# Kernel tuning notes

Hardware: AMD Instinct MI355X
Metric: run time of the kernel (lower is better)

## Reference

```python
import jax, jax.numpy as jnp
import numpy as np

T, N, H, G = 4, 100000, 128, 1024
LN2 = float(np.log(2.0))
EPS = 1e-5


def ssp(x):
    # shifted softplus: softplus(x) - softplus(0)
    return jax.nn.softplus(x) - LN2


def layernorm(x, g, b):
    m = jnp.mean(x, axis=-1, keepdims=True)
    v = jnp.var(x, axis=-1, keepdims=True)
    return (x - m) * jax.lax.rsqrt(v + EPS) * g + b


def mlp3(x, Ws, bs, gs, bts):
    # 3 stacked Linear -> LayerNorm -> SSP stages
    for i in range(3):
        x = ssp(layernorm(x @ Ws[i] + bs[i], gs[i], bts[i]))
    return x


def setup_inputs() -> dict:
    key = jax.random.key(0)
    ks = jax.random.split(key, 8)
    s = 1.0 / np.sqrt(H)
    batch = jnp.sort((jnp.arange(N, dtype=jnp.int64) * G) // N).astype(jnp.int32)
    return {
        "x_proc": jax.random.normal(ks[0], (T, N, H), jnp.float32),
        "x_enc": jax.random.normal(ks[1], (N, H), jnp.float32),
        "batch": batch,
        "pW": jax.random.normal(ks[2], (3, H, H), jnp.float32) * s,
        "pb": jnp.zeros((3, H), jnp.float32),
        "pg": jnp.ones((3, H), jnp.float32),
        "pbt": jnp.zeros((3, H), jnp.float32),
        "eW": jax.random.normal(ks[3], (3, H, H), jnp.float32) * s,
        "eb": jnp.zeros((3, H), jnp.float32),
        "eg": jnp.ones((3, H), jnp.float32),
        "ebt": jnp.zeros((3, H), jnp.float32),
        "wp": jax.random.normal(ks[4], (H, 1), jnp.float32) * s,
        "bp": jnp.zeros((1,), jnp.float32),
        "we": jax.random.normal(ks[5], (H, 1), jnp.float32) * s,
        "be": jnp.zeros((1,), jnp.float32),
    }


def reference(x_proc, x_enc, batch, pW, pb, pg, pbt, eW, eb, eg, ebt, wp, bp, we, be):
    h_proc = mlp3(x_proc, pW, pb, pg, pbt)          # [T, N, H]
    h_enc = mlp3(x_enc, eW, eb, eg, ebt)            # [N, H]
    seg = lambda z: jax.ops.segment_sum(z, batch, num_segments=G)
    pooled_proc = jax.vmap(seg)(h_proc)             # [T, G, H]
    pooled_enc = seg(h_enc)                         # [G, H]
    target = pooled_proc @ wp + bp + (pooled_enc @ we + be)[None]  # [T, G, 1]
    return target.reshape(-1, G)                    # [T, G]
```

## Files before the change

### kernel.cpp

```cpp
#include <hip/hip_runtime.h>
#include <hip/hip_bf16.h>

typedef unsigned short u16;
typedef unsigned int u32;
typedef __bf16 bf16x8 __attribute__((ext_vector_type(8)));
typedef float f32x16 __attribute__((ext_vector_type(16)));
typedef float f32x4 __attribute__((ext_vector_type(4)));
typedef float f32x2 __attribute__((ext_vector_type(2)));
typedef u32 u32x4 __attribute__((ext_vector_type(4)));

typedef struct { f32x2 h[2]; } f32x4p;
typedef struct { f32x2 h[8]; } f32x16p;

typedef __attribute__((address_space(1))) const u32 glb_u32;
typedef __attribute__((address_space(3))) u32 lds_u32;

#define NN 100000
#define NPROC_BLOCKS 3125
#define NENC_BLOCKS 782
#define LN2F 0.69314718055994530942f
#define LOG2EF 1.44269504088896340736f
#define CSTRIDE 1284

__device__ __forceinline__ u16 f2bf(float f) {
  u32 u = __float_as_uint(f);
  u32 r = u + 0x7fffu + ((u >> 16) & 1u);
  return (u16)(r >> 16);
}

__device__ __forceinline__ u32 pk2(float a, float b) {
  float2 f2; f2.x = a; f2.y = b;
  __hip_bfloat162 h = __float22bfloat162_rn(f2);
  u32 r;
  __builtin_memcpy(&r, &h, 4);
  return r;
}

__device__ __forceinline__ float l2p1e(float xp) {
  return __builtin_amdgcn_logf(1.0f + __builtin_amdgcn_exp2f(xp));
}

__global__ void prep_kernel(const float* __restrict__ pW, const float* __restrict__ eW,
                            const float* __restrict__ pb, const float* __restrict__ pg,
                            const float* __restrict__ pbt,
                            const float* __restrict__ eb, const float* __restrict__ eg,
                            const float* __restrict__ ebt,
                            const float* __restrict__ wp, const float* __restrict__ we,
                            const float* __restrict__ bp, const float* __restrict__ be,
                            u16* __restrict__ wt, float* __restrict__ cprep,
                            float* __restrict__ out) {
  int bx = blockIdx.x;
  int t = threadIdx.x;
  if (bx < 384) {
    int idx = bx * 256 + t;
    int m = idx >> 14;
    int within = idx & 16383;
    int r = within >> 7;
    int c = within & 127;
    int k = (((c >> 3) ^ (r & 15)) << 3) | (c & 7);
    const float* src = (m < 3) ? pW : eW;
    int ms = (m < 3) ? m : m - 3;
    float w = src[ms * 16384 + k * 128 + r];
    if (ms >= 1) w *= LN2F;
    wt[idx] = f2bf(w);
    if (idx < 4096) out[idx] = bp[0] + be[0];
  } else {
    int which = bx - 384;
    int net = which / 3;
    int s = which % 3;
    const float* W  = net ? eW : pW;
    const float* b  = net ? eb : pb;
    const float* g  = net ? eg : pg;
    const float* bt = net ? ebt : pbt;
    const float* wv = net ? we : wp;
    float* cp = cprep + net * CSTRIDE;
    __shared__ float red[128];

    int j = t & 127;
    int half = t >> 7;
    if (t < 128) {
      cp[(s * 3 + 1) * 128 + j] = g[s * 128 + j] * LOG2EF;
      cp[(s * 3 + 2) * 128 + j] = bt[s * 128 + j] * LOG2EF;
    }
    if (s == 0) {
      if (t < 128) {
        cp[0 * 128 + j] = b[j];
        cp[9 * 128 + j] = LN2F * wv[j];
      }
      if (t < 64) {
        float v = wv[t] + wv[t + 64];
        #pragma unroll
        for (int off = 1; off < 64; off <<= 1) v += __shfl_xor(v, off, 64);
        if (t == 0) cp[1280] = -LN2F * v;
      }
    } else {
      float part = 0.f;
      const float* Ws = W + s * 16384 + half * 64 * 128 + j;
      #pragma unroll 8
      for (int k = 0; k < 64; ++k) part += Ws[k * 128];
      if (half == 1) red[j] = part;
      __syncthreads();
      if (half == 0) {
        float cs = part + red[j];
        cp[(s * 3 + 0) * 128 + j] = b[s * 128 + j] - LN2F * cs;
      }
    }
  }
}

__global__ __launch_bounds__(256, 3)
void mlp_kernel(const float* __restrict__ x_proc, const float* __restrict__ x_enc,
                const u16* __restrict__ wt, const float* __restrict__ cprep,
                const int* __restrict__ batch, float* __restrict__ out) {
  __shared__ __align__(16) unsigned char wbuf[32768];
  __shared__ f32x4 cball[10][32];
  __shared__ float c0s;

  const bool is_proc = blockIdx.x < NPROC_BLOCKS;
  const int bid2 = is_proc ? blockIdx.x : blockIdx.x - NPROC_BLOCKS;
  const float* x = is_proc ? x_proc : x_enc;
  const unsigned char* wgb = (const unsigned char*)(is_proc ? wt : wt + 49152);
  const float* cp = cprep + (is_proc ? 0 : CSTRIDE);
  const int nrows = is_proc ? 400000 : 100000;

  const int tid = threadIdx.x;
  const int lane = tid & 63;
  const int wid = tid >> 6;
  const int l31 = lane & 31;
  const u32 hi = (u32)(lane >> 5);
  const int brow = bid2 * 128;

  auto issue_w = [&](int s_) {
    #pragma unroll
    for (int i = 0; i < 8; ++i) {
      const unsigned char* gp = wgb + s_ * 32768 + i * 4096 + tid * 16;
      unsigned char* lp = wbuf + i * 4096 + wid * 1024;
      __builtin_amdgcn_global_load_lds((const glb_u32*)(const void*)gp,
                                       (lds_u32*)(void*)lp, 16, 0, 0);
    }
  };

  issue_w(0);

  for (int i = tid; i < 320; i += 256)
    ((f32x4*)cball)[i] = *(const f32x4*)(cp + i * 4);
  if (tid == 0) c0s = cp[1280];

  const int rloc = wid * 32 + l31;
  const int grow = brow + rloc;
  const float* xr = x + (size_t)((grow < nrows) ? grow : (nrows - 1)) * 128 + (int)hi * 8;
  bf16x8 bfr[8];
  {
    f32x4 a[16];
    #pragma unroll
    for (int ks = 0; ks < 8; ++ks) {
      a[2 * ks]     = *(const f32x4*)(xr + ks * 16);
      a[2 * ks + 1] = *(const f32x4*)(xr + ks * 16 + 4);
    }
    #pragma unroll
    for (int ks = 0; ks < 8; ++ks) {
      u32x4 tq;
      tq.x = pk2(a[2 * ks][0], a[2 * ks][1]);
      tq.y = pk2(a[2 * ks][2], a[2 * ks][3]);
      tq.z = pk2(a[2 * ks + 1][0], a[2 * ks + 1][1]);
      tq.w = pk2(a[2 * ks + 1][2], a[2 * ks + 1][3]);
      bfr[ks] = __builtin_bit_cast(bf16x8, tq);
    }
  }

  float pfin = 0.0f;

  #pragma unroll
  for (int s = 0; s < 3; ++s) {
    __syncthreads();

    f32x16 acc[4];
    #pragma unroll
    for (int jf = 0; jf < 4; ++jf)
      #pragma unroll
      for (int q = 0; q < 4; ++q) {
        f32x4 b4 = cball[s * 3 + 0][jf * 8 + 2 * q + (int)hi];
        acc[jf][4 * q + 0] = b4[0];
        acc[jf][4 * q + 1] = b4[1];
        acc[jf][4 * q + 2] = b4[2];
        acc[jf][4 * q + 3] = b4[3];
      }

    #pragma unroll
    for (int ks = 0; ks < 8; ++ks) {
      int aoff = l31 * 256 + (((2 * ks + (int)hi) ^ (l31 & 15)) << 4);
      #pragma unroll
      for (int jf = 0; jf < 4; ++jf) {
        const bf16x8 afrag = *(const bf16x8*)(const void*)(wbuf + jf * 8192 + aoff);
        acc[jf] = __builtin_amdgcn_mfma_f32_32x32x16_bf16(afrag, bfr[ks], acc[jf], 0, 0, 0);
      }
      if (ks & 1) __builtin_amdgcn_sched_barrier(0);
    }

    if (s < 2) {
      __syncthreads();
      issue_w(s + 1);
    }

    f32x2 s1v = {0.f, 0.f}, s2v = {0.f, 0.f};
    #pragma unroll
    for (int jf = 0; jf < 4; ++jf) {
      f32x16p az = __builtin_bit_cast(f32x16p, acc[jf]);
      f32x2 p1 = {0.f, 0.f}, p2 = {0.f, 0.f};
      #pragma unroll
      for (int e = 0; e < 8; ++e) {
        f32x2 v = az.h[e];
        p1 += v;
        p2 = __builtin_elementwise_fma(v, v, p2);
      }
      s1v += p1; s2v += p2;
    }
    float s1 = s1v[0] + s1v[1];
    float s2 = s2v[0] + s2v[1];
    s1 += __shfl_xor(s1, 32, 64);
    s2 += __shfl_xor(s2, 32, 64);
    float mean = s1 * 0.0078125f;
    float var = s2 * 0.0078125f - mean * mean;
    float rstd = rsqrtf(var + 1e-5f);
    float nmr = -mean * rstd;
    const f32x2 rstd2 = {rstd, rstd};
    const f32x2 nmr2 = {nmr, nmr};

    if (s < 2) {
      #pragma unroll
      for (int ks = 0; ks < 8; ++ks) {
        int jf = ks >> 1, q0 = (ks & 1) << 1;
        f32x16p az = __builtin_bit_cast(f32x16p, acc[jf]);
        uint2 wq[2];
        #pragma unroll
        for (int qq = 0; qq < 2; ++qq) {
          int q = q0 + qq;
          f32x4p g = __builtin_bit_cast(f32x4p, cball[s * 3 + 1][jf * 8 + 2 * q + (int)hi]);
          f32x4p t = __builtin_bit_cast(f32x4p, cball[s * 3 + 2][jf * 8 + 2 * q + (int)hi]);
          f32x2 u0 = __builtin_elementwise_fma(az.h[2 * q + 0], rstd2, nmr2);
          f32x2 u1 = __builtin_elementwise_fma(az.h[2 * q + 1], rstd2, nmr2);
          f32x2 x0 = __builtin_elementwise_fma(u0, g.h[0], t.h[0]);
          f32x2 x1 = __builtin_elementwise_fma(u1, g.h[1], t.h[1]);
          wq[qq].x = pk2(l2p1e(x0[0]), l2p1e(x0[1]));
          wq[qq].y = pk2(l2p1e(x1[0]), l2p1e(x1[1]));
        }
        u32 sx = hi ? wq[0].x : wq[1].x;
        u32 sy = hi ? wq[0].y : wq[1].y;
        u32 rx = (u32)__shfl_xor((int)sx, 32, 64);
        u32 ry = (u32)__shfl_xor((int)sy, 32, 64);
        u32x4 tq;
        tq.x = hi ? rx : wq[0].x;
        tq.y = hi ? ry : wq[0].y;
        tq.z = hi ? wq[1].x : rx;
        tq.w = hi ? wq[1].y : ry;
        bfr[ks] = __builtin_bit_cast(bf16x8, tq);
      }
    } else {
      float pa = 0.f, pb2 = 0.f;
      #pragma unroll
      for (int jf = 0; jf < 4; ++jf) {
        f32x16p az = __builtin_bit_cast(f32x16p, acc[jf]);
        #pragma unroll
        for (int q = 0; q < 4; ++q) {
          f32x4 g4 = cball[7][jf * 8 + 2 * q + (int)hi];
          f32x4 t4 = cball[8][jf * 8 + 2 * q + (int)hi];
          f32x4 w4 = cball[9][jf * 8 + 2 * q + (int)hi];
          f32x4p g = __builtin_bit_cast(f32x4p, g4);
          f32x4p t = __builtin_bit_cast(f32x4p, t4);
          f32x2 u0 = __builtin_elementwise_fma(az.h[2 * q + 0], rstd2, nmr2);
          f32x2 u1 = __builtin_elementwise_fma(az.h[2 * q + 1], rstd2, nmr2);
          f32x2 x0 = __builtin_elementwise_fma(u0, g.h[0], t.h[0]);
          f32x2 x1 = __builtin_elementwise_fma(u1, g.h[1], t.h[1]);
          pa = __builtin_fmaf(l2p1e(x0[0]), w4[0], pa);
          pb2 = __builtin_fmaf(l2p1e(x0[1]), w4[1], pb2);
          pa = __builtin_fmaf(l2p1e(x1[0]), w4[2], pa);
          pb2 = __builtin_fmaf(l2p1e(x1[1]), w4[3], pb2);
        }
      }
      pfin = pa + pb2;
    }
  }

  pfin += __shfl_xor(pfin, 32, 64);
  if (grow < nrows) {
    pfin += c0s;
    int cell;
    if (is_proc) {
      int tt = grow / NN;
      cell = tt * 1024 + batch[grow - tt * NN];
    } else {
      cell = batch[grow];
    }
    int ca = __shfl(cell, 0, 32);
    int cz = __shfl(cell, 31, 32);
    if (ca == cz) {
      float r = pfin;
      #pragma unroll
      for (int off = 1; off < 32; off <<= 1) r += __shfl_xor(r, off, 64);
      if (hi == 0) {
        if (is_proc) {
          if (l31 == 0) atomicAdd(out + ca, r);
        } else {
          if (l31 < 4) atomicAdd(out + l31 * 1024 + ca, r);
        }
      }
    } else if (hi == 0) {
      if (is_proc) {
        atomicAdd(out + cell, pfin);
      } else {
        #pragma unroll
        for (int t2 = 0; t2 < 4; ++t2) atomicAdd(out + t2 * 1024 + cell, pfin);
      }
    }
  }
}

extern "C" void kernel_launch(void* const* d_in, const int* in_sizes, int n_in,
                              void* d_out, int out_size, void* d_ws, size_t ws_size,
                              hipStream_t stream) {
  const float* x_proc = (const float*)d_in[0];
  const float* x_enc  = (const float*)d_in[1];
  const int*   batch  = (const int*)d_in[2];
  const float* pW  = (const float*)d_in[3];
  const float* pb  = (const float*)d_in[4];
  const float* pg  = (const float*)d_in[5];
  const float* pbt = (const float*)d_in[6];
  const float* eW  = (const float*)d_in[7];
  const float* eb  = (const float*)d_in[8];
  const float* eg  = (const float*)d_in[9];
  const float* ebt = (const float*)d_in[10];
  const float* wp  = (const float*)d_in[11];
  const float* bp  = (const float*)d_in[12];
  const float* we  = (const float*)d_in[13];
  const float* be  = (const float*)d_in[14];

  float* out = (float*)d_out;
  u16* wt_ws = (u16*)d_ws;
  float* cprep = (float*)((char*)d_ws + 196608);

  prep_kernel<<<390, 256, 0, stream>>>(pW, eW, pb, pg, pbt, eb, eg, ebt,
                                       wp, we, bp, be, wt_ws, cprep, out);
  mlp_kernel<<<NPROC_BLOCKS + NENC_BLOCKS, 256, 0, stream>>>(
      x_proc, x_enc, wt_ws, cprep, batch, out);
}
```

Baseline: 144.2 us.

## Convert MLP kernel to persistent blocks with atomic tile counter

Launches a fixed number of persistent blocks (768 total, split between proc and enc) that fetch further 128-row tiles through a global atomic counter initialized in the prep kernel. This removes per-block launch overhead and the repeated per-block loading of constants, and balances work dynamically. The stage-0 weight reload is issued at the end of each tile while atomics are done, but x loads for the next tile are not prefetched ahead of compute, so latency may be exposed. It adds an extra global atomic and barrier per tile.

```diff
diff --git a/kernel.cpp b/kernel.cpp
--- a/kernel.cpp
+++ b/kernel.cpp
@@ -16,11 +16,14 @@
 typedef __attribute__((address_space(3))) u32 lds_u32;
 
 #define NN 100000
-#define NPROC_BLOCKS 3125
-#define NENC_BLOCKS 782
+#define NPROC_TILES 3125
+#define NENC_TILES 782
+#define NPROC_PBLK 614
+#define NENC_PBLK 154
 #define LN2F 0.69314718055994530942f
 #define LOG2EF 1.44269504088896340736f
 #define CSTRIDE 1284
+#define CNT_OFF 206880
 
 __device__ __forceinline__ u16 f2bf(float f) {
   u32 u = __float_as_uint(f);
@@ -48,7 +51,7 @@
                             const float* __restrict__ wp, const float* __restrict__ we,
                             const float* __restrict__ bp, const float* __restrict__ be,
                             u16* __restrict__ wt, float* __restrict__ cprep,
-                            float* __restrict__ out) {
+                            int* __restrict__ cnt, float* __restrict__ out) {
   int bx = blockIdx.x;
   int t = threadIdx.x;
   if (bx < 384) {
@@ -64,6 +67,7 @@
     if (ms >= 1) w *= LN2F;
     wt[idx] = f2bf(w);
     if (idx < 4096) out[idx] = bp[0] + be[0];
+    if (bx == 0 && t == 0) { cnt[0] = NPROC_PBLK; cnt[1] = NENC_PBLK; }
   } else {
     int which = bx - 384;
     int net = which / 3;
@@ -111,24 +115,27 @@
 __global__ __launch_bounds__(256, 3)
 void mlp_kernel(const float* __restrict__ x_proc, const float* __restrict__ x_enc,
                 const u16* __restrict__ wt, const float* __restrict__ cprep,
-                const int* __restrict__ batch, float* __restrict__ out) {
+                const int* __restrict__ batch, int* __restrict__ cnt,
+                float* __restrict__ out) {
   __shared__ __align__(16) unsigned char wbuf[32768];
   __shared__ f32x4 cball[10][32];
   __shared__ float c0s;
-
-  const bool is_proc = blockIdx.x < NPROC_BLOCKS;
-  const int bid2 = is_proc ? blockIdx.x : blockIdx.x - NPROC_BLOCKS;
+  __shared__ int sh_tn;
+
+  const bool is_proc = blockIdx.x < NPROC_PBLK;
+  const int bid2 = is_proc ? blockIdx.x : blockIdx.x - NPROC_PBLK;
   const float* x = is_proc ? x_proc : x_enc;
   const unsigned char* wgb = (const unsigned char*)(is_proc ? wt : wt + 49152);
   const float* cp = cprep + (is_proc ? 0 : CSTRIDE);
   const int nrows = is_proc ? 400000 : 100000;
+  const int ntiles = is_proc ? NPROC_TILES : NENC_TILES;
+  int* cntp = cnt + (is_proc ? 0 : 1);
 
   const int tid = threadIdx.x;
   const int lane = tid & 63;
   const int wid = tid >> 6;
   const int l31 = lane & 31;
   const u32 hi = (u32)(lane >> 5);
-  const int brow = bid2 * 128;
 
   auto issue_w = [&](int s_) {
     #pragma unroll
@@ -147,10 +154,12 @@
   if (tid == 0) c0s = cp[1280];
 
   const int rloc = wid * 32 + l31;
-  const int grow = brow + rloc;
-  const float* xr = x + (size_t)((grow < nrows) ? grow : (nrows - 1)) * 128 + (int)hi * 8;
+  int tile = bid2;
+  int grow = tile * 128 + rloc;
+
   bf16x8 bfr[8];
-  {
+  auto load_x = [&]() {
+    const float* xr = x + (size_t)((grow < nrows) ? grow : (nrows - 1)) * 128 + (int)hi * 8;
     f32x4 a[16];
     #pragma unroll
     for (int ks = 0; ks < 8; ++ks) {
@@ -166,152 +175,165 @@
       tq.w = pk2(a[2 * ks + 1][2], a[2 * ks + 1][3]);
       bfr[ks] = __builtin_bit_cast(bf16x8, tq);
     }
-  }
-
-  float pfin = 0.0f;
-
-  #pragma unroll
-  for (int s = 0; s < 3; ++s) {
-    __syncthreads();
-
-    f32x16 acc[4];
+  };
+  load_x();
+
+  for (;;) {
+    float pfin = 0.0f;
+
     #pragma unroll
-    for (int jf = 0; jf < 4; ++jf)
+    for (int s = 0; s < 3; ++s) {
+      __syncthreads();
+      if (s == 2 && tid == 0) sh_tn = atomicAdd(cntp, 1);
+
+      f32x16 acc[4];
       #pragma unroll
-      for (int q = 0; q < 4; ++q) {
-        f32x4 b4 = cball[s * 3 + 0][jf * 8 + 2 * q + (int)hi];
-        acc[jf][4 * q + 0] = b4[0];
-        acc[jf][4 * q + 1] = b4[1];
-        acc[jf][4 * q + 2] = b4[2];
-        acc[jf][4 * q + 3] = b4[3];
-      }
-
-    #pragma unroll
-    for (int ks = 0; ks < 8; ++ks) {
-      int aoff = l31 * 256 + (((2 * ks + (int)hi) ^ (l31 & 15)) << 4);
-      #pragma unroll
-      for (int jf = 0; jf < 4; ++jf) {
-        const bf16x8 afrag = *(const bf16x8*)(const void*)(wbuf + jf * 8192 + aoff);
-        acc[jf] = __builtin_amdgcn_mfma_f32_32x32x16_bf16(afrag, bfr[ks], acc[jf], 0, 0, 0);
-      }
-      if (ks & 1) __builtin_amdgcn_sched_barrier(0);
-    }
-
-    if (s < 2) {
-      __syncthreads();
-      issue_w(s + 1);
-    }
-
-    f32x2 s1v = {0.f, 0.f}, s2v = {0.f, 0.f};
-    #pragma unroll
-    for (int jf = 0; jf < 4; ++jf) {
-      f32x16p az = __builtin_bit_cast(f32x16p, acc[jf]);
-      f32x2 p1 = {0.f, 0.f}, p2 = {0.f, 0.f};
-      #pragma unroll
-      for (int e = 0; e < 8; ++e) {
-        f32x2 v = az.h[e];
-        p1 += v;
-        p2 = __builtin_elementwise_fma(v, v, p2);
-      }
-      s1v += p1; s2v += p2;
-    }
-    float s1 = s1v[0] + s1v[1];
-    float s2 = s2v[0] + s2v[1];
-    s1 += __shfl_xor(s1, 32, 64);
-    s2 += __shfl_xor(s2, 32, 64);
-    float mean = s1 * 0.0078125f;
-    float var = s2 * 0.0078125f - mean * mean;
-    float rstd = rsqrtf(var + 1e-5f);
-    float nmr = -mean * rstd;
-    const f32x2 rstd2 = {rstd, rstd};
-    const f32x2 nmr2 = {nmr, nmr};
-
-    if (s < 2) {
+      for (int jf = 0; jf < 4; ++jf)
+        #pragma unroll
+        for (int q = 0; q < 4; ++q) {
+          f32x4 b4 = cball[s * 3 + 0][jf * 8 + 2 * q + (int)hi];
+          acc[jf][4 * q + 0] = b4[0];
+          acc[jf][4 * q + 1] = b4[1];
+          acc[jf][4 * q + 2] = b4[2];
+          acc[jf][4 * q + 3] = b4[3];
+        }
+
       #pragma unroll
       for (int ks = 0; ks < 8; ++ks) {
-        int jf = ks >> 1, q0 = (ks & 1) << 1;
-        f32x16p az = __builtin_bit_cast(f32x16p, acc[jf]);
-        uint2 wq[2];
-        #pragma unroll
-        for (int qq = 0; qq < 2; ++qq) {
-          int q = q0 + qq;
-          f32x4p g = __builtin_bit_cast(f32x4p, cball[s * 3 + 1][jf * 8 + 2 * q + (int)hi]);
-          f32x4p t = __builtin_bit_cast(f32x4p, cball[s * 3 + 2][jf * 8 + 2 * q + (int)hi]);
-          f32x2 u0 = __builtin_elementwise_fma(az.h[2 * q + 0], rstd2, nmr2);
-          f32x2 u1 = __builtin_elementwise_fma(az.h[2 * q + 1], rstd2, nmr2);
-          f32x2 x0 = __builtin_elementwise_fma(u0, g.h[0], t.h[0]);
-          f32x2 x1 = __builtin_elementwise_fma(u1, g.h[1], t.h[1]);
-          wq[qq].x = pk2(l2p1e(x0[0]), l2p1e(x0[1]));
-          wq[qq].y = pk2(l2p1e(x1[0]), l2p1e(x1[1]));
-        }
-        u32 sx = hi ? wq[0].x : wq[1].x;
-        u32 sy = hi ? wq[0].y : wq[1].y;
-        u32 rx = (u32)__shfl_xor((int)sx, 32, 64);
-        u32 ry = (u32)__shfl_xor((int)sy, 32, 64);
-        u32x4 tq;
-        tq.x = hi ? rx : wq[0].x;
-        tq.y = hi ? ry : wq[0].y;
-        tq.z = hi ? wq[1].x : rx;
-        tq.w = hi ? wq[1].y : ry;
-        bfr[ks] = __builtin_bit_cast(bf16x8, tq);
-      }
-    } else {
-      float pa = 0.f, pb2 = 0.f;
+        int aoff = l31 * 256 + (((2 * ks + (int)hi) ^ (l31 & 15)) << 4);
+        #pragma unroll
+        for (int jf = 0; jf < 4; ++jf) {
+          const bf16x8 afrag = *(const bf16x8*)(const void*)(wbuf + jf * 8192 + aoff);
+          acc[jf] = __builtin_amdgcn_mfma_f32_32x32x16_bf16(afrag, bfr[ks], acc[jf], 0, 0, 0);
+        }
+        if (ks & 1) __builtin_amdgcn_sched_barrier(0);
+      }
+
+      if (s < 2) {
+        __syncthreads();
+        issue_w(s + 1);
+      }
+
+      f32x2 s1v = {0.f, 0.f}, s2v = {0.f, 0.f};
       #pragma unroll
       for (int jf = 0; jf < 4; ++jf) {
         f32x16p az = __builtin_bit_cast(f32x16p, acc[jf]);
-        #pragma unroll
-        for (int q = 0; q < 4; ++q) {
-          f32x4 g4 = cball[7][jf * 8 + 2 * q + (int)hi];
-          f32x4 t4 = cball[8][jf * 8 + 2 * q + (int)hi];
-          f32x4 w4 = cball[9][jf * 8 + 2 * q + (int)hi];
-          f32x4p g = __builtin_bit_cast(f32x4p, g4);
-          f32x4p t = __builtin_bit_cast(f32x4p, t4);
-          f32x2 u0 = __builtin_elementwise_fma(az.h[2 * q + 0], rstd2, nmr2);
-          f32x2 u1 = __builtin_elementwise_fma(az.h[2 * q + 1], rstd2, nmr2);
-          f32x2 x0 = __builtin_elementwise_fma(u0, g.h[0], t.h[0]);
-          f32x2 x1 = __builtin_elementwise_fma(u1, g.h[1], t.h[1]);
-          pa = __builtin_fmaf(l2p1e(x0[0]), w4[0], pa);
-          pb2 = __builtin_fmaf(l2p1e(x0[1]), w4[1], pb2);
-          pa = __builtin_fmaf(l2p1e(x1[0]), w4[2], pa);
-          pb2 = __builtin_fmaf(l2p1e(x1[1]), w4[3], pb2);
-        }
-      }
-      pfin = pa + pb2;
-    }
-  }
-
-  pfin += __shfl_xor(pfin, 32, 64);
-  if (grow < nrows) {
-    pfin += c0s;
-    int cell;
-    if (is_proc) {
-      int tt = grow / NN;
-      cell = tt * 1024 + batch[grow - tt * NN];
-    } else {
-      cell = batch[grow];
-    }
-    int ca = __shfl(cell, 0, 32);
-    int cz = __shfl(cell, 31, 32);
-    if (ca == cz) {
-      float r = pfin;
-      #pragma unroll
-      for (int off = 1; off < 32; off <<= 1) r += __shfl_xor(r, off, 64);
-      if (hi == 0) {
+        f32x2 p1 = {0.f, 0.f}, p2 = {0.f, 0.f};
+        #pragma unroll
+        for (int e = 0; e < 8; ++e) {
+          f32x2 v = az.h[e];
+          p1 += v;
+          p2 = __builtin_elementwise_fma(v, v, p2);
+        }
+        s1v += p1; s2v += p2;
+      }
+      float s1 = s1v[0] + s1v[1];
+      float s2 = s2v[0] + s2v[1];
+      s1 += __shfl_xor(s1, 32, 64);
+      s2 += __shfl_xor(s2, 32, 64);
+      float mean = s1 * 0.0078125f;
+      float var = s2 * 0.0078125f - mean * mean;
+      float rstd = rsqrtf(var + 1e-5f);
+      float nmr = -mean * rstd;
+      const f32x2 rstd2 = {rstd, rstd};
+      const f32x2 nmr2 = {nmr, nmr};
+
+      if (s < 2) {
+        #pragma unroll
+        for (int ks = 0; ks < 8; ++ks) {
+          int jf = ks >> 1, q0 = (ks & 1) << 1;
+          f32x16p az = __builtin_bit_cast(f32x16p, acc[jf]);
+          uint2 wq[2];
+          #pragma unroll
+          for (int qq = 0; qq < 2; ++qq) {
+            int q = q0 + qq;
+            f32x4p g = __builtin_bit_cast(f32x4p, cball[s * 3 + 1][jf * 8 + 2 * q + (int)hi]);
+            f32x4p t = __builtin_bit_cast(f32x4p, cball[s * 3 + 2][jf * 8 + 2 * q + (int)hi]);
+            f32x2 u0 = __builtin_elementwise_fma(az.h[2 * q + 0], rstd2, nmr2);
+            f32x2 u1 = __builtin_elementwise_fma(az.h[2 * q + 1], rstd2, nmr2);
+            f32x2 x0 = __builtin_elementwise_fma(u0, g.h[0], t.h[0]);
+            f32x2 x1 = __builtin_elementwise_fma(u1, g.h[1], t.h[1]);
+            wq[qq].x = pk2(l2p1e(x0[0]), l2p1e(x0[1]));
+            wq[qq].y = pk2(l2p1e(x1[0]), l2p1e(x1[1]));
+          }
+          u32 sx = hi ? wq[0].x : wq[1].x;
+          u32 sy = hi ? wq[0].y : wq[1].y;
+          u32 rx = (u32)__shfl_xor((int)sx, 32, 64);
+          u32 ry = (u32)__shfl_xor((int)sy, 32, 64);
+          u32x4 tq;
+          tq.x = hi ? rx : wq[0].x;
+          tq.y = hi ? ry : wq[0].y;
+          tq.z = hi ? wq[1].x : rx;
+          tq.w = hi ? wq[1].y : ry;
+          bfr[ks] = __builtin_bit_cast(bf16x8, tq);
+        }
+      } else {
+        float pa = 0.f, pb2 = 0.f;
+        #pragma unroll
+        for (int jf = 0; jf < 4; ++jf) {
+          f32x16p az = __builtin_bit_cast(f32x16p, acc[jf]);
+          #pragma unroll
+          for (int q = 0; q < 4; ++q) {
+            f32x4 g4 = cball[7][jf * 8 + 2 * q + (int)hi];
+            f32x4 t4 = cball[8][jf * 8 + 2 * q + (int)hi];
+            f32x4 w4 = cball[9][jf * 8 + 2 * q + (int)hi];
+            f32x4p g = __builtin_bit_cast(f32x4p, g4);
+            f32x4p t = __builtin_bit_cast(f32x4p, t4);
+            f32x2 u0 = __builtin_elementwise_fma(az.h[2 * q + 0], rstd2, nmr2);
+            f32x2 u1 = __builtin_elementwise_fma(az.h[2 * q + 1], rstd2, nmr2);
+            f32x2 x0 = __builtin_elementwise_fma(u0, g.h[0], t.h[0]);
+            f32x2 x1 = __builtin_elementwise_fma(u1, g.h[1], t.h[1]);
+            pa = __builtin_fmaf(l2p1e(x0[0]), w4[0], pa);
+            pb2 = __builtin_fmaf(l2p1e(x0[1]), w4[1], pb2);
+            pa = __builtin_fmaf(l2p1e(x1[0]), w4[2], pa);
+            pb2 = __builtin_fmaf(l2p1e(x1[1]), w4[3], pb2);
+          }
+        }
+        pfin = pa + pb2;
+      }
+    }
+
+    __syncthreads();
+    issue_w(0);
+
+    pfin += __shfl_xor(pfin, 32, 64);
+    if (grow < nrows) {
+      float pv = pfin + c0s;
+      int cell;
+      if (is_proc) {
+        int tt = grow / NN;
+        cell = tt * 1024 + batch[grow - tt * NN];
+      } else {
+        cell = batch[grow];
+      }
+      int ca = __shfl(cell, 0, 32);
+      int cz = __shfl(cell, 31, 32);
+      if (ca == cz) {
+        float r = pv;
+        #pragma unroll
+        for (int off = 1; off < 32; off <<= 1) r += __shfl_xor(r, off, 64);
+        if (hi == 0) {
+          if (is_proc) {
+            if (l31 == 0) atomicAdd(out + ca, r);
+          } else {
+            if (l31 < 4) atomicAdd(out + l31 * 1024 + ca, r);
+          }
+        }
+      } else if (hi == 0) {
         if (is_proc) {
-          if (l31 == 0) atomicAdd(out + ca, r);
+          atomicAdd(out + cell, pv);
         } else {
-          if (l31 < 4) atomicAdd(out + l31 * 1024 + ca, r);
-        }
-      }
-    } else if (hi == 0) {
-      if (is_proc) {
-        atomicAdd(out + cell, pfin);
-      } else {
-        #pragma unroll
-        for (int t2 = 0; t2 < 4; ++t2) atomicAdd(out + t2 * 1024 + cell, pfin);
-      }
-    }
+          #pragma unroll
+          for (int t2 = 0; t2 < 4; ++t2) atomicAdd(out + t2 * 1024 + cell, pv);
+        }
+      }
+    }
+
+    int tn = sh_tn;
+    if (tn >= ntiles) break;
+    tile = tn;
+    grow = tile * 128 + rloc;
+    load_x();
   }
 }
 
@@ -337,9 +359,10 @@
   float* out = (float*)d_out;
   u16* wt_ws = (u16*)d_ws;
   float* cprep = (float*)((char*)d_ws + 196608);
+  int* cnt = (int*)((char*)d_ws + CNT_OFF);
 
   prep_kernel<<<390, 256, 0, stream>>>(pW, eW, pb, pg, pbt, eb, eg, ebt,
-                                       wp, we, bp, be, wt_ws, cprep, out);
-  mlp_kernel<<<NPROC_BLOCKS + NENC_BLOCKS, 256, 0, stream>>>(
-      x_proc, x_enc, wt_ws, cprep, batch, out);
-}
+                                       wp, we, bp, be, wt_ws, cprep, cnt, out);
+  mlp_kernel<<<NPROC_PBLK + NENC_PBLK, 256, 0, stream>>>(
+      x_proc, x_enc, wt_ws, cprep, batch, cnt, out);
+}
```

New measurement: 185.1 us. +28.3%, slower.
